# Performance work log

Hardware: AMD Instinct MI355X
Metric: run time of the kernel (lower is better)

## Reference

```python
import jax, jax.numpy as jnp
import numpy as np

N = 50000      # nodes
E = 800000     # edges
IN, HID, OUT = 256, 256, 128
FCH = 32       # fc_hidden per embedding
VDIM = 2
FINAL = 2
NUM_EMB = 20


def setup_inputs() -> dict:
    key = jax.random.key(0)
    ks = jax.random.split(key, 16)
    s = 0.05
    return {
        "x": jax.random.normal(ks[0], (N, IN), jnp.float32),
        "edge_index": jax.random.randint(ks[1], (2, E), 0, N),
        "edge_cat": jax.random.randint(ks[2], (E, 2), 0, NUM_EMB),
        "edge_val": jax.random.normal(ks[3], (E, VDIM), jnp.float32),
        "W1": jax.random.normal(ks[4], (IN, HID), jnp.float32) * s,
        "b1": jnp.zeros((HID,), jnp.float32),
        "W2": jax.random.normal(ks[5], (HID, OUT), jnp.float32) * s,
        "b2": jnp.zeros((OUT,), jnp.float32),
        "emb0": jax.random.normal(ks[6], (NUM_EMB, FCH), jnp.float32) * s,
        "emb1": jax.random.normal(ks[7], (NUM_EMB, FCH), jnp.float32) * s,
        "fW1": jax.random.normal(ks[8], (OUT + 2 * FCH + VDIM, FINAL), jnp.float32) * s,
        "fb1": jnp.zeros((FINAL,), jnp.float32),
        "fW2": jax.random.normal(ks[9], (FINAL, 2), jnp.float32) * s,
        "fb2": jnp.zeros((2,), jnp.float32),
    }


def gcn_conv(h_in, W, b, src, dst, n):
    # PyG GCNConv: linear, add self-loops, symmetric D^-1/2 (A+I) D^-1/2 aggregation, bias.
    h = h_in @ W                                    # [N, F]
    ones = jnp.ones(src.shape[0], h.dtype)
    deg = jax.ops.segment_sum(ones, dst, num_segments=n) + 1.0  # +1 self-loop
    dinv = jax.lax.rsqrt(deg)                       # deg >= 1 so finite
    norm = dinv[src] * dinv[dst]                    # [E]
    agg = jax.ops.segment_sum(h[src] * norm[:, None], dst, num_segments=n)
    agg = agg + h * (dinv * dinv)[:, None]          # self-loop term, norm = dinv_i^2
    return agg + b


def reference(x, edge_index, edge_cat, edge_val,
              W1, b1, W2, b2, emb0, emb1, fW1, fb1, fW2, fb2):
    src, dst = edge_index[0], edge_index[1]
    n = x.shape[0]
    h = jax.nn.relu(gcn_conv(x, W1, b1, src, dst, n))
    h = gcn_conv(h, W2, b2, src, dst, n)            # [N, OUT]
    node2edge = h[src] - h[dst]                     # [E, OUT]
    ev = jnp.concatenate([edge_val, emb0[edge_cat[:, 0]], emb1[edge_cat[:, 1]]], axis=1)
    total = jnp.concatenate([node2edge, ev], axis=1)  # [E, OUT+2*FCH+VDIM]
    z = jax.nn.relu(total @ fW1 + fb1)              # dropout is identity in eval mode
    return z @ fW2 + fb2                            # [E, 2]
```

## Files before the change

kernel.cpp:

```cpp
#include <hip/hip_runtime.h>

#define NN 50000
#define EE 800000
#define NB ((NN + 1023) / 1024)
#define DEGB ((EE + 255) / 256)
#define GEMMB (2 * ((NN + 63) / 64))

typedef _Float16 half8v __attribute__((ext_vector_type(8)));
typedef _Float16 half4v __attribute__((ext_vector_type(4)));
typedef float f32x4 __attribute__((ext_vector_type(4)));

__global__ __launch_bounds__(256) void deg_prep(const int* __restrict__ dst,
                                                int* __restrict__ deg,
                                                int* __restrict__ epos,
                                                const float* __restrict__ W1,
                                                const float* __restrict__ W2,
                                                const float* __restrict__ fW1,
                                                const float* __restrict__ emb0,
                                                const float* __restrict__ emb1,
                                                _Float16* __restrict__ BT,
                                                float* __restrict__ Wft,
                                                float2* __restrict__ t0,
                                                float2* __restrict__ t1) {
    __shared__ float T[64][65];
    int b = blockIdx.x;
    int t = threadIdx.x;
    if (b < DEGB) {
        int e = b * 256 + t;
        if (e < EE) epos[e] = atomicAdd(&deg[dst[e]], 1);
    } else if (b < DEGB + 16) {
        int bb = b - DEGB;
        int k0 = (bb >> 2) * 64, n0 = (bb & 3) * 64;
#pragma unroll
        for (int i = 0; i < 16; ++i) {
            int r = i * 4 + (t >> 6), c = t & 63;
            T[r][c] = W1[(size_t)(k0 + r) * 256 + n0 + c];
        }
        __syncthreads();
#pragma unroll
        for (int i = 0; i < 16; ++i) {
            int n = i * 4 + (t >> 6), k = t & 63;
            BT[(size_t)(n0 + n) * 256 + k0 + k] = (_Float16)T[k][n];
        }
    } else {
        int k = t;
        float s0 = 0.f, s1 = 0.f;
        for (int m = 0; m < 128; ++m) {
            float wv = W2[(size_t)k * 128 + m];
            s0 += wv * fW1[m * 2 + 0];
            s1 += wv * fW1[m * 2 + 1];
        }
        Wft[k] = s0;
        Wft[256 + k] = s1;
        if (k < 20) {
            float a0 = 0.f, a1 = 0.f, b0 = 0.f, b1v = 0.f;
            for (int u = 0; u < 32; ++u) {
                float e0 = emb0[k * 32 + u], e1 = emb1[k * 32 + u];
                a0 += e0 * fW1[(130 + u) * 2 + 0];
                a1 += e0 * fW1[(130 + u) * 2 + 1];
                b0 += e1 * fW1[(162 + u) * 2 + 0];
                b1v += e1 * fW1[(162 + u) * 2 + 1];
            }
            t0[k] = make_float2(a0, a1);
            t1[k] = make_float2(b0, b1v);
        }
    }
}

__global__ __launch_bounds__(1024) void scan_partial(const int* __restrict__ deg,
                                                     int* __restrict__ rowptr,
                                                     int* __restrict__ bsum) {
    __shared__ int wsum[16];
    int tid = threadIdx.x, lane = tid & 63, w = tid >> 6;
    int idx = blockIdx.x * 1024 + tid;
    int v = (idx < NN) ? deg[idx] : 0;
    int x = v;
#pragma unroll
    for (int off = 1; off < 64; off <<= 1) {
        int t = __shfl_up(x, off, 64);
        if (lane >= off) x += t;
    }
    if (lane == 63) wsum[w] = x;
    __syncthreads();
    if (w == 0) {
        int s = (lane < 16) ? wsum[lane] : 0;
#pragma unroll
        for (int off = 1; off < 16; off <<= 1) {
            int t = __shfl_up(s, off, 64);
            if (lane >= off) s += t;
        }
        if (lane < 16) wsum[lane] = s;
    }
    __syncthreads();
    int wpre = (w == 0) ? 0 : wsum[w - 1];
    if (idx < NN) rowptr[idx] = wpre + (x - v);
    if (tid == 0) bsum[blockIdx.x] = wsum[15];
}

__global__ __launch_bounds__(256) void scan_add_dinv(int* __restrict__ rowptr,
                                                     const int* __restrict__ bsum,
                                                     const int* __restrict__ deg,
                                                     float* __restrict__ dinv) {
    __shared__ int pre[NB + 1];
    int t = threadIdx.x;
    if (t < 64) {
        int v = (t < NB) ? bsum[t] : 0;
        int x = v;
#pragma unroll
        for (int o = 1; o < 64; o <<= 1) {
            int y = __shfl_up(x, o, 64);
            if (t >= o) x += y;
        }
        if (t < NB) pre[t] = x - v;
        if (t == NB - 1) pre[NB] = x;
    }
    __syncthreads();
    int idx = blockIdx.x * 256 + t;
    if (idx < NN) {
        rowptr[idx] += pre[idx >> 10];
        dinv[idx] = rsqrtf((float)deg[idx] + 1.0f);
    }
    if (blockIdx.x == 0 && t == 0) rowptr[NN] = pre[NB];
}

__global__ __launch_bounds__(256) void gemm_fill(const float* __restrict__ A,
                                                 const _Float16* __restrict__ BT,
                                                 _Float16* __restrict__ C, int M,
                                                 const int* __restrict__ src,
                                                 const int* __restrict__ dst,
                                                 const int* __restrict__ rowptr,
                                                 const int* __restrict__ epos,
                                                 int* __restrict__ csr_src) {
    if (blockIdx.x >= GEMMB) {
        int e = (blockIdx.x - GEMMB) * 256 + threadIdx.x;
        if (e < EE) {
            int d = dst[e];
            csr_src[rowptr[d] + epos[e]] = src[e];
        }
        return;
    }
    __shared__ _Float16 Ah[2][64][40];
    __shared__ _Float16 Bh[2][128][40];
    int tid = threadIdx.x;
    int bm = (blockIdx.x >> 1) * 64, bn = (blockIdx.x & 1) * 128;
    int w = tid >> 6, l = tid & 63;
    int wr = w >> 1, wc = w & 1;
    int lr = l & 15, lg = l >> 4;
    int ar0 = tid >> 3, ac0 = tid & 7;
    int ar1 = (tid + 256) >> 3, ac1 = (tid + 256) & 7;
    int bn0 = tid >> 2, bk0 = tid & 3;
    int bn1 = (tid + 256) >> 2, bk1 = (tid + 256) & 3;
    f32x4 acc[2][4] = {};
    float4 aR0, aR1;
    half8v bR0, bR1;

    auto load_regs = [&](int k0) {
        int gm0 = bm + ar0, gm1 = bm + ar1;
        aR0 = (gm0 < M) ? *(const float4*)&A[(size_t)gm0 * 256 + k0 + ac0 * 4]
                        : make_float4(0.f, 0.f, 0.f, 0.f);
        aR1 = (gm1 < M) ? *(const float4*)&A[(size_t)gm1 * 256 + k0 + ac1 * 4]
                        : make_float4(0.f, 0.f, 0.f, 0.f);
        bR0 = *(const half8v*)&BT[(size_t)(bn + bn0) * 256 + k0 + bk0 * 8];
        bR1 = *(const half8v*)&BT[(size_t)(bn + bn1) * 256 + k0 + bk1 * 8];
    };
    auto store_lds = [&](int buf) {
        half4v h0, h1;
        h0[0] = (_Float16)aR0.x; h0[1] = (_Float16)aR0.y;
        h0[2] = (_Float16)aR0.z; h0[3] = (_Float16)aR0.w;
        h1[0] = (_Float16)aR1.x; h1[1] = (_Float16)aR1.y;
        h1[2] = (_Float16)aR1.z; h1[3] = (_Float16)aR1.w;
        *(half4v*)&Ah[buf][ar0][ac0 * 4] = h0;
        *(half4v*)&Ah[buf][ar1][ac1 * 4] = h1;
        *(half8v*)&Bh[buf][bn0][bk0 * 8] = bR0;
        *(half8v*)&Bh[buf][bn1][bk1 * 8] = bR1;
    };

    load_regs(0);
    store_lds(0);
    __syncthreads();
#pragma unroll
    for (int ks = 0; ks < 8; ++ks) {
        int cur = ks & 1;
        if (ks < 7) load_regs((ks + 1) * 32);
        half8v a[2], b[4];
#pragma unroll
        for (int mf = 0; mf < 2; ++mf)
            a[mf] = *(const half8v*)&Ah[cur][wr * 32 + mf * 16 + lr][lg * 8];
#pragma unroll
        for (int nf = 0; nf < 4; ++nf)
            b[nf] = *(const half8v*)&Bh[cur][wc * 64 + nf * 16 + lr][lg * 8];
#pragma unroll
        for (int mf = 0; mf < 2; ++mf)
#pragma unroll
            for (int nf = 0; nf < 4; ++nf)
                acc[mf][nf] = __builtin_amdgcn_mfma_f32_16x16x32_f16(a[mf], b[nf], acc[mf][nf], 0, 0, 0);
        if (ks < 7) {
            __syncthreads();
            store_lds(cur ^ 1);
            __syncthreads();
        }
    }
#pragma unroll
    for (int mf = 0; mf < 2; ++mf) {
#pragma unroll
        for (int reg = 0; reg < 4; ++reg) {
            int gr = bm + wr * 32 + mf * 16 + lg * 4 + reg;
            if (gr < M) {
#pragma unroll
                for (int nf = 0; nf < 4; ++nf)
                    C[(size_t)gr * 256 + bn + wc * 64 + nf * 16 + lr] =
                        (_Float16)acc[mf][nf][reg];
            }
        }
    }
}

__global__ __launch_bounds__(256) void gather_project(const _Float16* __restrict__ hs,
                                                      const int* __restrict__ rowptr,
                                                      const int* __restrict__ csr_src,
                                                      const float* __restrict__ dinv,
                                                      const float* __restrict__ b1,
                                                      const float* __restrict__ Wft,
                                                      float2* __restrict__ q) {
    int i = blockIdx.x * 4 + (threadIdx.x >> 6);
    int l = threadIdx.x & 63;
    int lf = l & 31, le = l >> 5;
    if (i >= NN) return;
    int start = rowptr[i], end = rowptr[i + 1];
    float acc[8] = {};
    int j = start;
    for (; j + 7 < end; j += 8) {
        int s0 = csr_src[j + 0 + le];
        int s1 = csr_src[j + 2 + le];
        int s2 = csr_src[j + 4 + le];
        int s3 = csr_src[j + 6 + le];
        float d0 = dinv[s0], d1 = dinv[s1], d2 = dinv[s2], d3 = dinv[s3];
        half8v v0 = *(const half8v*)(hs + (size_t)s0 * 256 + lf * 8);
        half8v v1 = *(const half8v*)(hs + (size_t)s1 * 256 + lf * 8);
        half8v v2 = *(const half8v*)(hs + (size_t)s2 * 256 + lf * 8);
        half8v v3 = *(const half8v*)(hs + (size_t)s3 * 256 + lf * 8);
#pragma unroll
        for (int u = 0; u < 8; ++u)
            acc[u] += (d0 * (float)v0[u] + d1 * (float)v1[u]) +
                      (d2 * (float)v2[u] + d3 * (float)v3[u]);
    }
    for (; j + le < end; j += 2) {
        int s = csr_src[j + le];
        float ds = dinv[s];
        half8v v = *(const half8v*)(hs + (size_t)s * 256 + lf * 8);
#pragma unroll
        for (int u = 0; u < 8; ++u) acc[u] += ds * (float)v[u];
    }
#pragma unroll
    for (int u = 0; u < 8; ++u) acc[u] += __shfl_xor(acc[u], 32, 64);
    float di = dinv[i];
    half8v sv = *(const half8v*)(hs + (size_t)i * 256 + lf * 8);
    float q0 = 0.f, q1 = 0.f;
#pragma unroll
    for (int u = 0; u < 8; ++u) {
        float o = fmaxf((acc[u] + di * (float)sv[u]) * di + b1[lf * 8 + u], 0.f);
        q0 += o * Wft[lf * 8 + u];
        q1 += o * Wft[256 + lf * 8 + u];
    }
#pragma unroll
    for (int off = 16; off > 0; off >>= 1) {
        q0 += __shfl_xor(q0, off, 64);
        q1 += __shfl_xor(q1, off, 64);
    }
    if (l == 0) q[i] = make_float2(q0 * di, q1 * di);
}

__global__ __launch_bounds__(256) void gather_gn(const float2* __restrict__ q,
                                                 const int* __restrict__ rowptr,
                                                 const int* __restrict__ csr_src,
                                                 const float* __restrict__ dinv,
                                                 float2* __restrict__ gn) {
    int i = blockIdx.x * blockDim.x + threadIdx.x;
    if (i >= NN) return;
    int start = rowptr[i], end = rowptr[i + 1];
    float a0 = 0.f, a1 = 0.f;
    for (int j = start; j < end; ++j) {
        float2 v = q[csr_src[j]];
        a0 += v.x;
        a1 += v.y;
    }
    float2 self = q[i];
    float di = dinv[i];
    gn[i] = make_float2((a0 + self.x) * di, (a1 + self.y) * di);
}

__global__ __launch_bounds__(256) void edge_out(const float2* __restrict__ gn,
                                                const int* __restrict__ src,
                                                const int* __restrict__ dst,
                                                const int2* __restrict__ ecat,
                                                const float2* __restrict__ ev,
                                                const float* __restrict__ fW1,
                                                const float2* __restrict__ t0,
                                                const float2* __restrict__ t1,
                                                const float* __restrict__ fb1,
                                                const float* __restrict__ fW2,
                                                const float* __restrict__ fb2,
                                                float2* __restrict__ out) {
    int e = blockIdx.x * blockDim.x + threadIdx.x;
    if (e >= EE) return;
    int s = src[e], d = dst[e];
    float2 gs = gn[s], gd = gn[d];
    int2 c = ecat[e];
    float2 v = ev[e];
    float2 e0 = t0[c.x], e1 = t1[c.y];
    float z0 = gs.x - gd.x + v.x * fW1[128 * 2 + 0] + v.y * fW1[129 * 2 + 0] + e0.x + e1.x;
    float z1 = gs.y - gd.y + v.x * fW1[128 * 2 + 1] + v.y * fW1[129 * 2 + 1] + e0.y + e1.y;
    float y0 = fmaxf(z0 + fb1[0], 0.f);
    float y1 = fmaxf(z1 + fb1[1], 0.f);
    out[e] = make_float2(y0 * fW2[0] + y1 * fW2[2] + fb2[0],
                         y0 * fW2[1] + y1 * fW2[3] + fb2[1]);
}

extern "C" void kernel_launch(void* const* d_in, const int* in_sizes, int n_in,
                              void* d_out, int out_size, void* d_ws, size_t ws_size,
                              hipStream_t stream) {
    const float* x    = (const float*)d_in[0];
    const int*   eidx = (const int*)d_in[1];
    const int*   src  = eidx;
    const int*   dst  = eidx + EE;
    const int*   ecat = (const int*)d_in[2];
    const float* ev   = (const float*)d_in[3];
    const float* W1   = (const float*)d_in[4];
    const float* b1   = (const float*)d_in[5];
    const float* W2   = (const float*)d_in[6];
    const float* emb0 = (const float*)d_in[8];
    const float* emb1 = (const float*)d_in[9];
    const float* fW1  = (const float*)d_in[10];
    const float* fb1  = (const float*)d_in[11];
    const float* fW2  = (const float*)d_in[12];
    const float* fb2  = (const float*)d_in[13];
    float* out = (float*)d_out;

    char* ws = (char*)d_ws;
    size_t off = 0;
    auto alloc = [&](size_t bytes) {
        void* p = ws + off;
        off = (off + bytes + 255) & ~(size_t)255;
        return p;
    };
    int*      deg     = (int*)alloc((size_t)NN * 4);
    float*    dinv    = (float*)alloc((size_t)NN * 4);
    int*      rowptr  = (int*)alloc((size_t)(NN + 1) * 4);
    int*      bsum    = (int*)alloc((size_t)NB * 4);
    int*      epos    = (int*)alloc((size_t)EE * 4);
    int*      csr_src = (int*)alloc((size_t)EE * 4);
    _Float16* W1T     = (_Float16*)alloc((size_t)256 * 256 * 2);
    _Float16* h1s     = (_Float16*)alloc((size_t)NN * 256 * 2);
    float2*   q       = (float2*)alloc((size_t)NN * 8);
    float2*   gn      = (float2*)alloc((size_t)NN * 8);
    float*    Wft     = (float*)alloc(512 * 4);
    float2*   t0      = (float2*)alloc(20 * 8);
    float2*   t1      = (float2*)alloc(20 * 8);

    hipMemsetAsync(deg, 0, (size_t)NN * 4, stream);

    deg_prep<<<DEGB + 17, 256, 0, stream>>>(dst, deg, epos, W1, W2, fW1, emb0, emb1,
                                            W1T, Wft, t0, t1);

    scan_partial<<<NB, 1024, 0, stream>>>(deg, rowptr, bsum);
    scan_add_dinv<<<(NN + 255) / 256, 256, 0, stream>>>(rowptr, bsum, deg, dinv);

    gemm_fill<<<GEMMB + DEGB, 256, 0, stream>>>(x, W1T, h1s, NN,
                                                src, dst, rowptr, epos, csr_src);

    gather_project<<<(NN + 3) / 4, 256, 0, stream>>>(
        h1s, rowptr, csr_src, dinv, b1, Wft, q);
    gather_gn<<<(NN + 255) / 256, 256, 0, stream>>>(q, rowptr, csr_src, dinv, gn);
    edge_out<<<DEGB, 256, 0, stream>>>(
        gn, src, dst, (const int2*)ecat, (const float2*)ev,
        fW1, t0, t1, fb1, fW2, fb2, (float2*)out);
}
```

Baseline: 164.1 us.

## Pre-convert x to padded fp16 and stage GEMM tiles via direct global-to-LDS loads

Adds a conversion pass inside deg_prep that writes x as a zero-padded fp16 buffer. The layer-1 GEMM then loads A and B tiles straight into LDS with global_load_lds, dropping the register staging, in-loop fp32-to-fp16 conversion, double buffering and row bounds checks. The cost is an extra full read of x plus a write and re-read of a 25 MB fp16 copy. The GEMM loop also becomes single-buffered with no padding in LDS, so load latency is exposed each k-step and the fragment reads may hit bank conflicts.

New measurement: 165.0 us. No clear change (+0.6%).

```diff
diff --git a/kernel.cpp b/kernel.cpp
--- a/kernel.cpp
+++ b/kernel.cpp
@@ -1,18 +1,28 @@
 #include <hip/hip_runtime.h>
 
 #define NN 50000
+#define XPAD 50048
 #define EE 800000
 #define NB ((NN + 1023) / 1024)
 #define DEGB ((EE + 255) / 256)
-#define GEMMB (2 * ((NN + 63) / 64))
+#define NCVT (XPAD / 16)
+#define GEMMB (2 * (XPAD / 64))
 
 typedef _Float16 half8v __attribute__((ext_vector_type(8)));
 typedef _Float16 half4v __attribute__((ext_vector_type(4)));
 typedef float f32x4 __attribute__((ext_vector_type(4)));
 
+__device__ __forceinline__ void gload16(const _Float16* g, _Float16* l) {
+    __builtin_amdgcn_global_load_lds(
+        (const __attribute__((address_space(1))) unsigned int*)g,
+        (__attribute__((address_space(3))) unsigned int*)l, 16, 0, 0);
+}
+
 __global__ __launch_bounds__(256) void deg_prep(const int* __restrict__ dst,
                                                 int* __restrict__ deg,
                                                 int* __restrict__ epos,
+                                                const float* __restrict__ x,
+                                                _Float16* __restrict__ xh,
                                                 const float* __restrict__ W1,
                                                 const float* __restrict__ W2,
                                                 const float* __restrict__ fW1,
@@ -28,8 +38,30 @@
     if (b < DEGB) {
         int e = b * 256 + t;
         if (e < EE) epos[e] = atomicAdd(&deg[dst[e]], 1);
-    } else if (b < DEGB + 16) {
-        int bb = b - DEGB;
+    } else if (b < DEGB + NCVT) {
+        int b2 = b - DEGB;
+        int row = b2 * 16 + (t >> 4);
+        int col = (t & 15) * 16;
+        half8v h0, h1;
+        if (row < NN) {
+            const float4* xp = (const float4*)&x[(size_t)row * 256 + col];
+            float4 v0 = xp[0], v1 = xp[1], v2 = xp[2], v3 = xp[3];
+            h0[0] = (_Float16)v0.x; h0[1] = (_Float16)v0.y;
+            h0[2] = (_Float16)v0.z; h0[3] = (_Float16)v0.w;
+            h0[4] = (_Float16)v1.x; h0[5] = (_Float16)v1.y;
+            h0[6] = (_Float16)v1.z; h0[7] = (_Float16)v1.w;
+            h1[0] = (_Float16)v2.x; h1[1] = (_Float16)v2.y;
+            h1[2] = (_Float16)v2.z; h1[3] = (_Float16)v2.w;
+            h1[4] = (_Float16)v3.x; h1[5] = (_Float16)v3.y;
+            h1[6] = (_Float16)v3.z; h1[7] = (_Float16)v3.w;
+        } else {
+            h0 = (half8v)(_Float16)0.f;
+            h1 = (half8v)(_Float16)0.f;
+        }
+        *(half8v*)&xh[(size_t)row * 256 + col] = h0;
+        *(half8v*)&xh[(size_t)row * 256 + col + 8] = h1;
+    } else if (b < DEGB + NCVT + 16) {
+        int bb = b - DEGB - NCVT;
         int k0 = (bb >> 2) * 64, n0 = (bb & 3) * 64;
 #pragma unroll
         for (int i = 0; i < 16; ++i) {
@@ -123,7 +155,7 @@
     if (blockIdx.x == 0 && t == 0) rowptr[NN] = pre[NB];
 }
 
-__global__ __launch_bounds__(256) void gemm_fill(const float* __restrict__ A,
+__global__ __launch_bounds__(256) void gemm_fill(const _Float16* __restrict__ Axh,
                                                  const _Float16* __restrict__ BT,
                                                  _Float16* __restrict__ C, int M,
                                                  const int* __restrict__ src,
@@ -139,66 +171,41 @@
         }
         return;
     }
-    __shared__ _Float16 Ah[2][64][40];
-    __shared__ _Float16 Bh[2][128][40];
+    __shared__ _Float16 Ah[64 * 32];
+    __shared__ _Float16 Bh[128 * 32];
     int tid = threadIdx.x;
     int bm = (blockIdx.x >> 1) * 64, bn = (blockIdx.x & 1) * 128;
     int w = tid >> 6, l = tid & 63;
     int wr = w >> 1, wc = w & 1;
     int lr = l & 15, lg = l >> 4;
-    int ar0 = tid >> 3, ac0 = tid & 7;
-    int ar1 = (tid + 256) >> 3, ac1 = (tid + 256) & 7;
-    int bn0 = tid >> 2, bk0 = tid & 3;
-    int bn1 = (tid + 256) >> 2, bk1 = (tid + 256) & 3;
+    const _Float16* gA = Axh + (size_t)(bm + (tid >> 2)) * 256 + (tid & 3) * 8;
+    const _Float16* gB0 = BT + (size_t)(bn + (tid >> 2)) * 256 + (tid & 3) * 8;
+    const _Float16* gB1 = BT + (size_t)(bn + ((tid + 256) >> 2)) * 256 + (tid & 3) * 8;
+    _Float16* lA = Ah + tid * 8;
+    _Float16* lB0 = Bh + tid * 8;
+    _Float16* lB1 = Bh + (tid + 256) * 8;
     f32x4 acc[2][4] = {};
-    float4 aR0, aR1;
-    half8v bR0, bR1;
-
-    auto load_regs = [&](int k0) {
-        int gm0 = bm + ar0, gm1 = bm + ar1;
-        aR0 = (gm0 < M) ? *(const float4*)&A[(size_t)gm0 * 256 + k0 + ac0 * 4]
-                        : make_float4(0.f, 0.f, 0.f, 0.f);
-        aR1 = (gm1 < M) ? *(const float4*)&A[(size_t)gm1 * 256 + k0 + ac1 * 4]
-                        : make_float4(0.f, 0.f, 0.f, 0.f);
-        bR0 = *(const half8v*)&BT[(size_t)(bn + bn0) * 256 + k0 + bk0 * 8];
-        bR1 = *(const half8v*)&BT[(size_t)(bn + bn1) * 256 + k0 + bk1 * 8];
-    };
-    auto store_lds = [&](int buf) {
-        half4v h0, h1;
-        h0[0] = (_Float16)aR0.x; h0[1] = (_Float16)aR0.y;
-        h0[2] = (_Float16)aR0.z; h0[3] = (_Float16)aR0.w;
-        h1[0] = (_Float16)aR1.x; h1[1] = (_Float16)aR1.y;
-        h1[2] = (_Float16)aR1.z; h1[3] = (_Float16)aR1.w;
-        *(half4v*)&Ah[buf][ar0][ac0 * 4] = h0;
-        *(half4v*)&Ah[buf][ar1][ac1 * 4] = h1;
-        *(half8v*)&Bh[buf][bn0][bk0 * 8] = bR0;
-        *(half8v*)&Bh[buf][bn1][bk1 * 8] = bR1;
-    };
-
-    load_regs(0);
-    store_lds(0);
-    __syncthreads();
+
 #pragma unroll
     for (int ks = 0; ks < 8; ++ks) {
-        int cur = ks & 1;
-        if (ks < 7) load_regs((ks + 1) * 32);
+        int k0 = ks * 32;
+        gload16(gA + k0, lA);
+        gload16(gB0 + k0, lB0);
+        gload16(gB1 + k0, lB1);
+        __syncthreads();
         half8v a[2], b[4];
 #pragma unroll
         for (int mf = 0; mf < 2; ++mf)
-            a[mf] = *(const half8v*)&Ah[cur][wr * 32 + mf * 16 + lr][lg * 8];
+            a[mf] = *(const half8v*)&Ah[(wr * 32 + mf * 16 + lr) * 32 + lg * 8];
 #pragma unroll
         for (int nf = 0; nf < 4; ++nf)
-            b[nf] = *(const half8v*)&Bh[cur][wc * 64 + nf * 16 + lr][lg * 8];
+            b[nf] = *(const half8v*)&Bh[(wc * 64 + nf * 16 + lr) * 32 + lg * 8];
 #pragma unroll
         for (int mf = 0; mf < 2; ++mf)
 #pragma unroll
             for (int nf = 0; nf < 4; ++nf)
                 acc[mf][nf] = __builtin_amdgcn_mfma_f32_16x16x32_f16(a[mf], b[nf], acc[mf][nf], 0, 0, 0);
-        if (ks < 7) {
-            __syncthreads();
-            store_lds(cur ^ 1);
-            __syncthreads();
-        }
+        if (ks < 7) __syncthreads();
     }
 #pragma unroll
     for (int mf = 0; mf < 2; ++mf) {
@@ -350,6 +357,7 @@
     int*      epos    = (int*)alloc((size_t)EE * 4);
     int*      csr_src = (int*)alloc((size_t)EE * 4);
     _Float16* W1T     = (_Float16*)alloc((size_t)256 * 256 * 2);
+    _Float16* xh      = (_Float16*)alloc((size_t)XPAD * 256 * 2);
     _Float16* h1s     = (_Float16*)alloc((size_t)NN * 256 * 2);
     float2*   q       = (float2*)alloc((size_t)NN * 8);
     float2*   gn      = (float2*)alloc((size_t)NN * 8);
@@ -359,13 +367,14 @@
 
     hipMemsetAsync(deg, 0, (size_t)NN * 4, stream);
 
-    deg_prep<<<DEGB + 17, 256, 0, stream>>>(dst, deg, epos, W1, W2, fW1, emb0, emb1,
-                                            W1T, Wft, t0, t1);
+    deg_prep<<<DEGB + NCVT + 17, 256, 0, stream>>>(dst, deg, epos, x, xh,
+                                                   W1, W2, fW1, emb0, emb1,
+                                                   W1T, Wft, t0, t1);
 
     scan_partial<<<NB, 1024, 0, stream>>>(deg, rowptr, bsum);
     scan_add_dinv<<<(NN + 255) / 256, 256, 0, stream>>>(rowptr, bsum, deg, dinv);
 
-    gemm_fill<<<GEMMB + DEGB, 256, 0, stream>>>(x, W1T, h1s, NN,
+    gemm_fill<<<GEMMB + DEGB, 256, 0, stream>>>(xh, W1T, h1s, NN,
                                                 src, dst, rowptr, epos, csr_src);
 
     gather_project<<<(NN + 3) / 4, 256, 0, stream>>>(
```
